# Performance work log

Hardware: AMD Instinct MI355X
Metric: run time of the kernel (lower is better)

The kernel has to match this reference:

```python
import jax, jax.numpy as jnp
import numpy as np

N = 4194304  # number of sampled points (flattened)
W = 32       # hidden width
IN_PTS, IN_VIEWS = 3, 3


def setup_inputs() -> dict:
    key = jax.random.key(0)
    ks = jax.random.split(key, 13)
    def lin(k, fan_in, fan_out):
        # torch nn.Linear default init: U(-1/sqrt(fan_in), 1/sqrt(fan_in))
        bound = 1.0 / np.sqrt(fan_in)
        kw, kb = jax.random.split(k)
        w = jax.random.uniform(kw, (fan_in, fan_out), jnp.float32, -bound, bound)
        b = jax.random.uniform(kb, (fan_out,), jnp.float32, -bound, bound)
        return w, b
    x = jax.random.normal(ks[0], (N, IN_PTS + IN_VIEWS), jnp.float32)
    w0, b0 = lin(ks[1], IN_PTS, W)          # pts_linears[0]
    w1, b1 = lin(ks[2], W, W)               # pts_linears[1]
    wf, bf = lin(ks[3], W, W)               # feature_linear
    ws, bs = lin(ks[4], W, 1)               # sigma_linear
    wv, bv = lin(ks[5], IN_VIEWS + W, W)    # view_linears[0]
    wr, br = lin(ks[6], W, 3)               # rgb_linear
    return {"x": x, "w0": w0, "b0": b0, "w1": w1, "b1": b1,
            "wf": wf, "bf": bf, "ws": ws, "bs": bs,
            "wv": wv, "bv": bv, "wr": wr, "br": br}


def reference(x, w0, b0, w1, b1, wf, bf, ws, bs, wv, bv, wr, br):
    pts, views = x[..., :IN_PTS], x[..., IN_PTS:]
    h = jax.nn.relu(pts @ w0 + b0)
    h = jax.nn.relu(h @ w1 + b1)
    sigma = h @ ws + bs                     # [N, 1]
    feature = h @ wf + bf                   # [N, W]
    h = jnp.concatenate([feature, views], axis=-1)  # [N, W+3]
    h = jax.nn.relu(h @ wv + bv)
    rgb = h @ wr + br                       # [N, 3]
    return jnp.concatenate([rgb, sigma], axis=-1)   # [N, 4]
```

## Files before the change

kernel.cpp:

```cpp
#include <hip/hip_runtime.h>


#define NPTS   4194304
#define NT32   (NPTS / 32)

typedef _Float16 f16;
typedef _Float16 f16x2 __attribute__((ext_vector_type(2)));
typedef _Float16 f16x8 __attribute__((ext_vector_type(8)));
typedef __fp16   h16x2 __attribute__((ext_vector_type(2)));
typedef float    f32x16 __attribute__((ext_vector_type(16)));

union H8 { f16x8 v; unsigned u[4]; };

static __device__ __forceinline__ unsigned pkrtz(float a, float b) {
    return __builtin_bit_cast(unsigned, __builtin_amdgcn_cvt_pkrtz(a, b));
}
static __device__ __forceinline__ unsigned relu2(unsigned w) {
    f16x2 h = __builtin_bit_cast(f16x2, w);
    f16x2 z = (f16x2)(f16)0.f;
    return __builtin_bit_cast(unsigned, __builtin_elementwise_max(h, z));
}
static __device__ __forceinline__ float fdot2(unsigned a, unsigned b, float c) {
    return __builtin_amdgcn_fdot2(__builtin_bit_cast(h16x2, a),
                                  __builtin_bit_cast(h16x2, b), c, false);
}

#define MFMA32(A, B, C) __builtin_amdgcn_mfma_f32_32x32x16_f16((A), (B), (C), 0, 0, 0)

__global__ __launch_bounds__(256, 3) void kilonerf_r19(
    const float* __restrict__ x,
    const float* __restrict__ w0, const float* __restrict__ b0,
    const float* __restrict__ w1, const float* __restrict__ b1,
    const float* __restrict__ wf, const float* __restrict__ bf,
    const float* __restrict__ ws, const float* __restrict__ bs,
    const float* __restrict__ wv, const float* __restrict__ bv,
    const float* __restrict__ wr, const float* __restrict__ br,
    float* __restrict__ out)
{
    const int lane = threadIdx.x & 63;
    const int m  = lane & 31;
    const int hi = lane >> 5;

    int sj[8], row[16];
#pragma unroll
    for (int j = 0; j < 8; ++j)  sj[j]  = (j & 3) + 8 * (j >> 2) + 4 * hi;
#pragma unroll
    for (int r = 0; r < 16; ++r) row[r] = (r & 3) + 8 * (r >> 2) + 4 * hi;

    f32x16 zf;
#pragma unroll
    for (int r = 0; r < 16; ++r) zf[r] = 0.f;

    float bve = bv[m];
#pragma unroll 8
    for (int t = 0; t < 32; ++t) bve = fmaf(wv[t * 32 + m], bf[t], bve);

    f16x8 afw1, afw2, bwv1, bwv2;
#pragma unroll
    for (int j = 0; j < 8; ++j) {
        const int k = sj[j];
        afw1[j] = (f16)wf[m * 32 + k];
        afw2[j] = (f16)wf[m * 32 + 16 + k];
        bwv1[j] = (f16)wv[k * 32 + m];
        bwv2[j] = (f16)wv[(16 + k) * 32 + m];
    }
    f32x16 dwc = MFMA32(afw1, bwv1, zf);
    dwc = MFMA32(afw2, bwv2, dwc);
    f16x8 awclo, awchi;
#pragma unroll
    for (int j = 0; j < 8; ++j) {
        awclo[j] = (f16)dwc[j];
        awchi[j] = (f16)dwc[8 + j];
    }

    f16x8 aw0x, awv2x, aw1lo, aw1hi, awrlo, awrhi;
#pragma unroll
    for (int j = 0; j < 8; ++j) {
        const int k = sj[j];
        aw0x[j]  = (k < 3) ? (f16)w0[k * 32 + m]
                  : (k == 3 ? (f16)b0[m] : (f16)0.f);
        awv2x[j] = (k >= 4 && k < 7) ? (f16)wv[(32 + (k - 4)) * 32 + m]
                  : (k == 7 ? (f16)bve : (f16)0.f);
        aw1lo[j] = (f16)w1[k * 32 + m];
        aw1hi[j] = (f16)w1[(16 + k) * 32 + m];
        awrlo[j] = (m < 3) ? (f16)wr[k * 3 + m] : (f16)0.f;
        awrhi[j] = (m < 3) ? (f16)wr[(16 + k) * 3 + m] : (f16)0.f;
    }

    unsigned wspk[8];
#pragma unroll
    for (int w = 0; w < 8; ++w)
        wspk[w] = pkrtz(ws[row[2 * w]], ws[row[2 * w + 1]]);

    f32x16 b1c;
#pragma unroll
    for (int r = 0; r < 16; ++r) b1c[r] = b1[row[r]];

    const float br0 = br[0], br1 = br[1], br2 = br[2], bs0 = bs[0];

    const int wslot  = blockIdx.x * 4 + (threadIdx.x >> 6);
    const int nslots = gridDim.x * 4;

    float2 cx0, cx1, cx2;
    {
        const float2* xp2 = reinterpret_cast<const float2*>(
            x + (size_t)(wslot * 32 + m) * 6);
        cx0 = xp2[0]; cx1 = xp2[1]; cx2 = xp2[2];
    }

    for (int tile = wslot; tile < NT32; tile += nslots) {
        int np = tile + nslots; if (np >= NT32) np = wslot;
        const float2* xn = reinterpret_cast<const float2*>(
            x + (size_t)(np * 32 + m) * 6);
        float2 nx0 = xn[0], nx1 = xn[1], nx2 = xn[2];

        const float fa = hi ? cx1.y : cx0.x;
        const float fb = hi ? cx2.x : cx0.y;
        const float fc = hi ? cx2.y : cx1.x;
        H8 bx;
        bx.u[0] = pkrtz(fa, fb);
        bx.u[1] = pkrtz(fc, 1.0f);
        bx.u[2] = 0u;
        bx.u[3] = 0u;

        f32x16 c0 = MFMA32(aw0x, bx.v, zf);
        f32x16 cv = MFMA32(awv2x, bx.v, zf);

        H8 blo, bhi;
        blo.u[0] = relu2(pkrtz(c0[0], c0[1]));
        blo.u[1] = relu2(pkrtz(c0[2], c0[3]));
        blo.u[2] = relu2(pkrtz(c0[4], c0[5]));
        blo.u[3] = relu2(pkrtz(c0[6], c0[7]));
        bhi.u[0] = relu2(pkrtz(c0[8], c0[9]));
        bhi.u[1] = relu2(pkrtz(c0[10], c0[11]));
        bhi.u[2] = relu2(pkrtz(c0[12], c0[13]));
        bhi.u[3] = relu2(pkrtz(c0[14], c0[15]));

        f32x16 p0 = MFMA32(aw1lo, blo.v, b1c);
        f32x16 p1 = MFMA32(aw1hi, bhi.v, zf);
        f32x16 c1 = p0 + p1;

        blo.u[0] = relu2(pkrtz(c1[0], c1[1]));
        blo.u[1] = relu2(pkrtz(c1[2], c1[3]));
        blo.u[2] = relu2(pkrtz(c1[4], c1[5]));
        blo.u[3] = relu2(pkrtz(c1[6], c1[7]));
        bhi.u[0] = relu2(pkrtz(c1[8], c1[9]));
        bhi.u[1] = relu2(pkrtz(c1[10], c1[11]));
        bhi.u[2] = relu2(pkrtz(c1[12], c1[13]));
        bhi.u[3] = relu2(pkrtz(c1[14], c1[15]));

        float s0 = 0.f, s1 = 0.f;
#pragma unroll
        for (int w = 0; w < 4; ++w) {
            s0 = fdot2(blo.u[w], wspk[w], s0);
            s1 = fdot2(bhi.u[w], wspk[4 + w], s1);
        }
        float sg = s0 + s1;
        sg += __shfl_xor(sg, 32);

        f32x16 q0 = MFMA32(awclo, blo.v, cv);
        f32x16 q1 = MFMA32(awchi, bhi.v, zf);
        f32x16 cc = q0 + q1;

        blo.u[0] = relu2(pkrtz(cc[0], cc[1]));
        blo.u[1] = relu2(pkrtz(cc[2], cc[3]));
        blo.u[2] = relu2(pkrtz(cc[4], cc[5]));
        blo.u[3] = relu2(pkrtz(cc[6], cc[7]));
        bhi.u[0] = relu2(pkrtz(cc[8], cc[9]));
        bhi.u[1] = relu2(pkrtz(cc[10], cc[11]));
        bhi.u[2] = relu2(pkrtz(cc[12], cc[13]));
        bhi.u[3] = relu2(pkrtz(cc[14], cc[15]));

        f32x16 r0 = MFMA32(awrlo, blo.v, zf);
        f32x16 r1 = MFMA32(awrhi, bhi.v, zf);

        if (hi == 0) {
            float4 o = make_float4(r0[0] + r1[0] + br0,
                                   r0[1] + r1[1] + br1,
                                   r0[2] + r1[2] + br2, sg + bs0);
            *reinterpret_cast<float4*>(out + (size_t)(tile * 32 + m) * 4) = o;
        }

        cx0 = nx0; cx1 = nx1; cx2 = nx2;
    }
}

extern "C" void kernel_launch(void* const* d_in, const int* in_sizes, int n_in,
                              void* d_out, int out_size, void* d_ws, size_t ws_size,
                              hipStream_t stream) {
    const float* x  = (const float*)d_in[0];
    const float* w0 = (const float*)d_in[1];
    const float* b0 = (const float*)d_in[2];
    const float* w1 = (const float*)d_in[3];
    const float* b1 = (const float*)d_in[4];
    const float* wf = (const float*)d_in[5];
    const float* bf = (const float*)d_in[6];
    const float* ws = (const float*)d_in[7];
    const float* bs = (const float*)d_in[8];
    const float* wv = (const float*)d_in[9];
    const float* bv = (const float*)d_in[10];
    const float* wr = (const float*)d_in[11];
    const float* br = (const float*)d_in[12];
    float* out = (float*)d_out;

    dim3 block(256);
    dim3 grid(2048);
    kilonerf_r19<<<grid, block, 0, stream>>>(x, w0, b0, w1, b1, wf, bf,
                                             ws, bs, wv, bv, wr, br, out);
}
```

Baseline: 60.20 us.

## Software-pipeline first-layer MFMAs one tile ahead and chain MFMA accumulators

The first-layer and view MFMAs for the next tile are now issued inside the current iteration, and x loads are prefetched two tiles ahead, so MFMA latency and load latency overlap with the current tile's dependent chain. Paired MFMAs now accumulate through the C operand instead of being summed with separate vector adds. Launch bounds rise to 4 blocks per CU and the loop is unrolled by 2. In exchange, more accumulator registers stay live, which could cause spills under the tighter occupancy bound.

```diff
diff --git a/kernel.cpp b/kernel.cpp
--- a/kernel.cpp
+++ b/kernel.cpp
@@ -27,7 +27,7 @@
 
 #define MFMA32(A, B, C) __builtin_amdgcn_mfma_f32_32x32x16_f16((A), (B), (C), 0, 0, 0)
 
-__global__ __launch_bounds__(256, 3) void kilonerf_r19(
+__global__ __launch_bounds__(256, 4) void kilonerf_r20(
     const float* __restrict__ x,
     const float* __restrict__ w0, const float* __restrict__ b0,
     const float* __restrict__ w1, const float* __restrict__ b1,
@@ -101,44 +101,65 @@
     const int wslot  = blockIdx.x * 4 + (threadIdx.x >> 6);
     const int nslots = gridDim.x * 4;
 
-    float2 cx0, cx1, cx2;
+    f32x16 c0c, cvc;
     {
         const float2* xp2 = reinterpret_cast<const float2*>(
             x + (size_t)(wslot * 32 + m) * 6);
-        cx0 = xp2[0]; cx1 = xp2[1]; cx2 = xp2[2];
-    }
-
+        const float2 a0 = xp2[0], a1 = xp2[1], a2 = xp2[2];
+        const float fa = hi ? a1.y : a0.x;
+        const float fb = hi ? a2.x : a0.y;
+        const float fc = hi ? a2.y : a1.x;
+        H8 bxc;
+        bxc.u[0] = pkrtz(fa, fb);
+        bxc.u[1] = pkrtz(fc, 1.0f);
+        bxc.u[2] = 0u;
+        bxc.u[3] = 0u;
+        c0c = MFMA32(aw0x, bxc.v, zf);
+        cvc = MFMA32(awv2x, bxc.v, zf);
+    }
+    float2 nx0, nx1, nx2;
+    {
+        int pn = wslot + nslots; if (pn >= NT32) pn = wslot;
+        const float2* xp2 = reinterpret_cast<const float2*>(
+            x + (size_t)(pn * 32 + m) * 6);
+        nx0 = xp2[0]; nx1 = xp2[1]; nx2 = xp2[2];
+    }
+
+#pragma unroll 2
     for (int tile = wslot; tile < NT32; tile += nslots) {
-        int np = tile + nslots; if (np >= NT32) np = wslot;
-        const float2* xn = reinterpret_cast<const float2*>(
-            x + (size_t)(np * 32 + m) * 6);
-        float2 nx0 = xn[0], nx1 = xn[1], nx2 = xn[2];
-
-        const float fa = hi ? cx1.y : cx0.x;
-        const float fb = hi ? cx2.x : cx0.y;
-        const float fc = hi ? cx2.y : cx1.x;
-        H8 bx;
-        bx.u[0] = pkrtz(fa, fb);
-        bx.u[1] = pkrtz(fc, 1.0f);
-        bx.u[2] = 0u;
-        bx.u[3] = 0u;
-
-        f32x16 c0 = MFMA32(aw0x, bx.v, zf);
-        f32x16 cv = MFMA32(awv2x, bx.v, zf);
+        int tn  = tile + nslots; if (tn  >= NT32) tn  = wslot;
+        int tn2 = tn   + nslots; if (tn2 >= NT32) tn2 = wslot;
+
+        const float fa = hi ? nx1.y : nx0.x;
+        const float fb = hi ? nx2.x : nx0.y;
+        const float fc = hi ? nx2.y : nx1.x;
+        H8 bxn;
+        bxn.u[0] = pkrtz(fa, fb);
+        bxn.u[1] = pkrtz(fc, 1.0f);
+        bxn.u[2] = 0u;
+        bxn.u[3] = 0u;
+
+        {
+            const float2* xq = reinterpret_cast<const float2*>(
+                x + (size_t)(tn2 * 32 + m) * 6);
+            nx0 = xq[0]; nx1 = xq[1]; nx2 = xq[2];
+        }
 
         H8 blo, bhi;
-        blo.u[0] = relu2(pkrtz(c0[0], c0[1]));
-        blo.u[1] = relu2(pkrtz(c0[2], c0[3]));
-        blo.u[2] = relu2(pkrtz(c0[4], c0[5]));
-        blo.u[3] = relu2(pkrtz(c0[6], c0[7]));
-        bhi.u[0] = relu2(pkrtz(c0[8], c0[9]));
-        bhi.u[1] = relu2(pkrtz(c0[10], c0[11]));
-        bhi.u[2] = relu2(pkrtz(c0[12], c0[13]));
-        bhi.u[3] = relu2(pkrtz(c0[14], c0[15]));
-
-        f32x16 p0 = MFMA32(aw1lo, blo.v, b1c);
-        f32x16 p1 = MFMA32(aw1hi, bhi.v, zf);
-        f32x16 c1 = p0 + p1;
+        blo.u[0] = relu2(pkrtz(c0c[0], c0c[1]));
+        blo.u[1] = relu2(pkrtz(c0c[2], c0c[3]));
+        blo.u[2] = relu2(pkrtz(c0c[4], c0c[5]));
+        blo.u[3] = relu2(pkrtz(c0c[6], c0c[7]));
+        bhi.u[0] = relu2(pkrtz(c0c[8], c0c[9]));
+        bhi.u[1] = relu2(pkrtz(c0c[10], c0c[11]));
+        bhi.u[2] = relu2(pkrtz(c0c[12], c0c[13]));
+        bhi.u[3] = relu2(pkrtz(c0c[14], c0c[15]));
+
+        f32x16 c0n = MFMA32(aw0x, bxn.v, zf);
+        f32x16 cvn = MFMA32(awv2x, bxn.v, zf);
+
+        f32x16 c1 = MFMA32(aw1lo, blo.v, b1c);
+        c1 = MFMA32(aw1hi, bhi.v, c1);
 
         blo.u[0] = relu2(pkrtz(c1[0], c1[1]));
         blo.u[1] = relu2(pkrtz(c1[2], c1[3]));
@@ -158,9 +179,8 @@
         float sg = s0 + s1;
         sg += __shfl_xor(sg, 32);
 
-        f32x16 q0 = MFMA32(awclo, blo.v, cv);
-        f32x16 q1 = MFMA32(awchi, bhi.v, zf);
-        f32x16 cc = q0 + q1;
+        f32x16 cc = MFMA32(awclo, blo.v, cvc);
+        cc = MFMA32(awchi, bhi.v, cc);
 
         blo.u[0] = relu2(pkrtz(cc[0], cc[1]));
         blo.u[1] = relu2(pkrtz(cc[2], cc[3]));
@@ -171,17 +191,17 @@
         bhi.u[2] = relu2(pkrtz(cc[12], cc[13]));
         bhi.u[3] = relu2(pkrtz(cc[14], cc[15]));
 
-        f32x16 r0 = MFMA32(awrlo, blo.v, zf);
-        f32x16 r1 = MFMA32(awrhi, bhi.v, zf);
+        f32x16 cr = MFMA32(awrlo, blo.v, zf);
+        cr = MFMA32(awrhi, bhi.v, cr);
 
         if (hi == 0) {
-            float4 o = make_float4(r0[0] + r1[0] + br0,
-                                   r0[1] + r1[1] + br1,
-                                   r0[2] + r1[2] + br2, sg + bs0);
+            float4 o = make_float4(cr[0] + br0, cr[1] + br1,
+                                   cr[2] + br2, sg + bs0);
             *reinterpret_cast<float4*>(out + (size_t)(tile * 32 + m) * 4) = o;
         }
 
-        cx0 = nx0; cx1 = nx1; cx2 = nx2;
+        c0c = c0n;
+        cvc = cvn;
     }
 }
 
@@ -205,6 +225,6 @@
 
     dim3 block(256);
     dim3 grid(2048);
-    kilonerf_r19<<<grid, block, 0, stream>>>(x, w0, b0, w1, b1, wf, bf,
+    kilonerf_r20<<<grid, block, 0, stream>>>(x, w0, b0, w1, b1, wf, bf,
                                              ws, bs, wv, bv, wr, br, out);
 }
```

Result: faster. 57.56 us (-4.4%).
